# Kernel optimization log

Measured on AMD Instinct MI355X. Metric: run time of the kernel, lower is better.

Reference implementation:

```python
import jax, jax.numpy as jnp
import numpy as np

D_ATT = 256
D_GROUP = 32
N_GROUP = D_ATT // D_GROUP


def setup_inputs() -> dict:
    key = jax.random.key(0)
    ks = jax.random.split(key, 6)
    B, L = 4, 512
    import math
    s = 1.0 / math.sqrt(D_ATT)
    return {
        "x": jax.random.normal(ks[0], (B, L, D_ATT), dtype=jnp.float32),
        "Wq": jax.random.normal(ks[1], (D_ATT, D_ATT), dtype=jnp.float32) * s * 0.06,
        "Wk": jax.random.normal(ks[2], (D_ATT, D_ATT), dtype=jnp.float32) * s * 0.06,
        "Wv": jax.random.normal(ks[3], (D_ATT, D_ATT), dtype=jnp.float32) * s * 0.06,
        "w_mlp": jax.random.normal(ks[4], (D_GROUP,), dtype=jnp.float32) * 0.1,
        "b_mlp": jax.random.normal(ks[5], (1,), dtype=jnp.float32) * 0.1,
    }


def reference(x, Wq, Wk, Wv, w_mlp, b_mlp):
    B, L, d_att = x.shape
    G, Dg = N_GROUP, D_GROUP
    # nn.Linear(bias=False): y = x @ W.T
    Q = x @ Wq.T  # (B, L, d_att)
    K = x @ Wk.T
    V = x @ Wv.T
    Qg = Q.reshape(B, L, 1, G, Dg)
    Kg = K.reshape(B, 1, L, G, Dg)
    # group_MLP: ReLU -> Linear(Dg, 1) -> ReLU, applied to Q-K diff
    # diff: (B, Lq, Lk, G, Dg) -- the huge intermediate a fused kernel would avoid
    diff = Qg - Kg
    attn = jnp.einsum('bqkgd,d->bqkg', jax.nn.relu(diff), w_mlp) + b_mlp[0]
    attn = jax.nn.relu(attn)
    # positional_adding_bias=0, positional_multiplying_bias=1 (defaults), no mask
    attn = jax.nn.softmax(attn, axis=2)  # softmax over key positions
    # NOTE: original views V as (B, L, d_group, n_group) -- asymmetric grouping, kept faithful
    Vg = V.reshape(B, L, Dg, G)
    out = jnp.einsum('bqkg,bkdg->bqdg', attn, Vg)  # (B, Lq, Dg, G)
    return out.reshape(B, L, d_att)
```

## Files before the change

### kernel.cpp

```cpp
#include <hip/hip_runtime.h>

typedef float f32x2 __attribute__((ext_vector_type(2)));
typedef float f32x4 __attribute__((ext_vector_type(4)));
typedef short bf16x8 __attribute__((ext_vector_type(8)));

#define LL 512
#define M_ROWS 2048
#define KC 768

#if __has_builtin(__builtin_amdgcn_exp2f)
#define EXP2F __builtin_amdgcn_exp2f
#else
#define EXP2F exp2f
#endif
#define LOG2E 1.44269504088896340736f

__device__ __forceinline__ float quad_swap1(float x) {
    return __int_as_float(__builtin_amdgcn_mov_dpp(__float_as_int(x), 0xB1, 0xF, 0xF, true));
}
__device__ __forceinline__ float quad_swap2(float x) {
    return __int_as_float(__builtin_amdgcn_mov_dpp(__float_as_int(x), 0x4E, 0xF, 0xF, true));
}

__device__ __forceinline__ unsigned short bf16_rtne(float x) {
    unsigned u = __float_as_uint(x);
    return (unsigned short)((u + 0x7fffu + ((u >> 16) & 1u)) >> 16);
}
__device__ __forceinline__ float bf16_to_f(unsigned short h) {
    return __uint_as_float((unsigned)h << 16);
}

__global__ __launch_bounds__(64) void split_bf16(
    const float* __restrict__ X, const float* __restrict__ Wq,
    const float* __restrict__ Wk, const float* __restrict__ Wv,
    unsigned short* __restrict__ Xc, unsigned short* __restrict__ Wc)
{
    const int row = blockIdx.x;
    const int t = threadIdx.x;
    const float* src;
    unsigned short* hi1; unsigned short* hi2; unsigned short* lo1;
    if (row < M_ROWS) {
        src = X + (size_t)row * 256;
        hi1 = Xc + (size_t)row * KC;
        hi2 = hi1 + 256;
        lo1 = hi1 + 512;
    } else {
        const int n = row - M_ROWS;
        const int mat = n >> 8, c = n & 255;
        const int srow = (mat == 2) ? (((c & 31) << 3) | (c >> 5)) : c;
        src = (mat == 0 ? Wq : (mat == 1 ? Wk : Wv)) + (size_t)srow * 256;
        hi1 = Wc + (size_t)n * KC;
        lo1 = hi1 + 256;
        hi2 = hi1 + 512;
    }
    const f32x4 v = *(const f32x4*)(src + t * 4);
    ushort4 h, l;
    h.x = bf16_rtne(v.x); h.y = bf16_rtne(v.y); h.z = bf16_rtne(v.z); h.w = bf16_rtne(v.w);
    l.x = bf16_rtne(v.x - bf16_to_f(h.x));
    l.y = bf16_rtne(v.y - bf16_to_f(h.y));
    l.z = bf16_rtne(v.z - bf16_to_f(h.z));
    l.w = bf16_rtne(v.w - bf16_to_f(h.w));
    *(ushort4*)(hi1 + t * 4) = h;
    *(ushort4*)(hi2 + t * 4) = h;
    *(ushort4*)(lo1 + t * 4) = l;
}

__global__ __launch_bounds__(64) void qkv_mfma(
    const unsigned short* __restrict__ Xc, const unsigned short* __restrict__ Wc,
    float* __restrict__ Y)
{
    const int bid = blockIdx.x;
    const int m0 = (bid & 31) * 64;
    const int n0 = (bid >> 5) * 64;
    const int l = threadIdx.x;
    const int lr = l & 15;
    const int lk = (l >> 4) * 8;

    size_t aoff[4], boff[4];
#pragma unroll
    for (int i = 0; i < 4; ++i) {
        aoff[i] = (size_t)(m0 + i * 16 + lr) * KC + lk;
        boff[i] = (size_t)(n0 + i * 16 + lr) * KC + lk;
    }

    f32x4 acc[4][4];
#pragma unroll
    for (int i = 0; i < 4; ++i)
#pragma unroll
        for (int j = 0; j < 4; ++j) acc[i][j] = (f32x4){0.f, 0.f, 0.f, 0.f};

    bf16x8 A0[4], B0[4], A1[4], B1[4];
#pragma unroll
    for (int i = 0; i < 4; ++i) {
        A0[i] = *(const bf16x8*)(Xc + aoff[i]);
        B0[i] = *(const bf16x8*)(Wc + boff[i]);
    }

#pragma unroll 1
    for (int it = 0; it < 24; it += 2) {
        const int ks1 = (it + 1) * 32;
#pragma unroll
        for (int i = 0; i < 4; ++i) {
            A1[i] = *(const bf16x8*)(Xc + aoff[i] + ks1);
            B1[i] = *(const bf16x8*)(Wc + boff[i] + ks1);
        }
#pragma unroll
        for (int ai = 0; ai < 4; ++ai)
#pragma unroll
            for (int bi = 0; bi < 4; ++bi)
                acc[ai][bi] = __builtin_amdgcn_mfma_f32_16x16x32_bf16(
                    A0[ai], B0[bi], acc[ai][bi], 0, 0, 0);
        if (it + 2 < 24) {
            const int ks2 = (it + 2) * 32;
#pragma unroll
            for (int i = 0; i < 4; ++i) {
                A0[i] = *(const bf16x8*)(Xc + aoff[i] + ks2);
                B0[i] = *(const bf16x8*)(Wc + boff[i] + ks2);
            }
        }
#pragma unroll
        for (int ai = 0; ai < 4; ++ai)
#pragma unroll
            for (int bi = 0; bi < 4; ++bi)
                acc[ai][bi] = __builtin_amdgcn_mfma_f32_16x16x32_bf16(
                    A1[ai], B1[bi], acc[ai][bi], 0, 0, 0);
    }

    const int mat = n0 >> 8;
    float* Yb = Y + (size_t)mat * M_ROWS * 256;
#pragma unroll
    for (int ai = 0; ai < 4; ++ai)
#pragma unroll
        for (int bi = 0; bi < 4; ++bi) {
            const int col = (n0 & 255) + bi * 16 + lr;
#pragma unroll
            for (int r = 0; r < 4; ++r) {
                const int row = m0 + ai * 16 + (l >> 4) * 4 + r;
                Yb[(size_t)row * 256 + col] = acc[ai][bi][r];
            }
        }
}

__global__ __launch_bounds__(512, 4) void attn_fused(
    const float* __restrict__ Y,
    const float* __restrict__ w_mlp, const float* __restrict__ b_mlp,
    float* __restrict__ out)
{
    const float* Qm = Y;
    const float* Km = Y + (size_t)M_ROWS * 256;
    const float* Vt = Y + (size_t)2 * M_ROWS * 256;

    const int bid = blockIdx.x;
    const int b = bid & 3;
    const int q0 = (bid >> 2) * 4;

    const int t = threadIdx.x;
    const int dh = t & 3;
    const int p = t >> 5;
    const int lane32 = t & 31;
    const int g = lane32 >> 2;

    __shared__ float accbuf[16][32][37];

    const int doff = g * 32 + dh * 8;
    const float bias4 = b_mlp[0] * (LOG2E * 0.25f);

    f32x2 w2[4];
    {
        f32x4 wa = *(const f32x4*)(w_mlp + dh * 8);
        f32x4 wb = *(const f32x4*)(w_mlp + dh * 8 + 4);
        wa *= LOG2E; wb *= LOG2E;
        w2[0] = __builtin_shufflevector(wa, wa, 0, 1);
        w2[1] = __builtin_shufflevector(wa, wa, 2, 3);
        w2[2] = __builtin_shufflevector(wb, wb, 0, 1);
        w2[3] = __builtin_shufflevector(wb, wb, 2, 3);
    }

    f32x2 qr2[4][4];
#pragma unroll
    for (int q = 0; q < 4; ++q) {
        const float* qp = Qm + ((size_t)(b * LL) + q0 + q) * 256 + doff;
        f32x4 qa = *(const f32x4*)qp;
        f32x4 qb = *(const f32x4*)(qp + 4);
        qr2[q][0] = __builtin_shufflevector(qa, qa, 0, 1);
        qr2[q][1] = __builtin_shufflevector(qa, qa, 2, 3);
        qr2[q][2] = __builtin_shufflevector(qb, qb, 0, 1);
        qr2[q][3] = __builtin_shufflevector(qb, qb, 2, 3);
    }

    f32x2 acc2[4][4];
#pragma unroll
    for (int q = 0; q < 4; ++q)
#pragma unroll
        for (int j = 0; j < 4; ++j) acc2[q][j] = (f32x2){0.f, 0.f};
    float l[4] = {0.f, 0.f, 0.f, 0.f};

    const float* kptr = Km + ((size_t)(b * LL) + p) * 256 + doff;
    const float* vptr = Vt + ((size_t)(b * LL) + p) * 256 + doff;

    auto compute = [&](f32x4 ka, f32x4 kb, f32x4 va, f32x4 vb) {
        f32x2 k2[4] = {__builtin_shufflevector(ka, ka, 0, 1),
                       __builtin_shufflevector(ka, ka, 2, 3),
                       __builtin_shufflevector(kb, kb, 0, 1),
                       __builtin_shufflevector(kb, kb, 2, 3)};
        f32x2 v2[4] = {__builtin_shufflevector(va, va, 0, 1),
                       __builtin_shufflevector(va, va, 2, 3),
                       __builtin_shufflevector(vb, vb, 0, 1),
                       __builtin_shufflevector(vb, vb, 2, 3)};
        const f32x2 z2 = {0.f, 0.f};
#pragma unroll
        for (int q = 0; q < 4; ++q) {
            f32x2 s2 = {bias4, 0.f};
#pragma unroll
            for (int j = 0; j < 4; ++j) {
                f32x2 d2 = qr2[q][j] - k2[j];
                f32x2 r2 = __builtin_elementwise_max(d2, z2);
                s2 += w2[j] * r2;
            }
            float s = s2.x + s2.y;
            s += quad_swap1(s);
            s += quad_swap2(s);
            s = fmaxf(s, 0.f);
            const float e = EXP2F(s);
            l[q] += e;
            const f32x2 e2 = {e, e};
#pragma unroll
            for (int j = 0; j < 4; ++j) acc2[q][j] += e2 * v2[j];
        }
    };

    f32x4 ka = *(const f32x4*)kptr, kb = *(const f32x4*)(kptr + 4);
    f32x4 va = *(const f32x4*)vptr, vb = *(const f32x4*)(vptr + 4);
#pragma unroll 1
    for (int i = 0; i < 31; ++i) {
        kptr += 16 * 256; vptr += 16 * 256;
        f32x4 ka2 = *(const f32x4*)kptr, kb2 = *(const f32x4*)(kptr + 4);
        f32x4 va2 = *(const f32x4*)vptr, vb2 = *(const f32x4*)(vptr + 4);
        compute(ka, kb, va, vb);
        ka = ka2; kb = kb2; va = va2; vb = vb2;
    }
    compute(ka, kb, va, vb);

    {
        float* rowp = &accbuf[p][lane32][0];
#pragma unroll
        for (int qq = 0; qq < 4; ++qq)
#pragma unroll
            for (int j = 0; j < 4; ++j)
                *(f32x2*)(rowp + qq * 8 + j * 2) = acc2[qq][j];
        if (dh == 0) {
#pragma unroll
            for (int qq = 0; qq < 4; ++qq) accbuf[p][lane32][32 + qq] = l[qq];
        }
    }
    __syncthreads();

    const int c_o = t & 255;
    const int g_o = c_o & 7, d_o = c_o >> 3;
    const int rowb = g_o * 4 + (d_o >> 3);
    const int colb = d_o & 7;
    const int qsel = t >> 8;
#pragma unroll
    for (int h = 0; h < 2; ++h) {
        const int qh = qsel + 2 * h;
        float s = 0.f, ls = 0.f;
#pragma unroll
        for (int pp = 0; pp < 16; ++pp) {
            s  += accbuf[pp][rowb][qh * 8 + colb];
            ls += accbuf[pp][g_o * 4][32 + qh];
        }
        out[((size_t)(b * LL) + q0 + qh) * 256 + c_o] = s / ls;
    }
}

extern "C" void kernel_launch(void* const* d_in, const int* in_sizes, int n_in,
                              void* d_out, int out_size, void* d_ws, size_t ws_size,
                              hipStream_t stream) {
    (void)in_sizes; (void)n_in; (void)out_size; (void)ws_size;
    const float* x     = (const float*)d_in[0];
    const float* Wq    = (const float*)d_in[1];
    const float* Wk    = (const float*)d_in[2];
    const float* Wv    = (const float*)d_in[3];
    const float* w_mlp = (const float*)d_in[4];
    const float* b_mlp = (const float*)d_in[5];
    float* outp = (float*)d_out;

    float* Y = (float*)d_ws;
    unsigned short* Xc = (unsigned short*)((char*)d_ws + (size_t)6291456);
    unsigned short* Wc = (unsigned short*)((char*)d_ws + (size_t)6291456 + 3145728);

    split_bf16<<<dim3(M_ROWS + 768), 64, 0, stream>>>(x, Wq, Wk, Wv, Xc, Wc);
    qkv_mfma<<<dim3(384), 64, 0, stream>>>(Xc, Wc, Y);
    attn_fused<<<dim3(512), 512, 0, stream>>>(Y, w_mlp, b_mlp, outp);
}
```

Before: 124.3 us.

## Stage K/V tiles through double-buffered shared memory with coalesced loads

Instead of each thread loading its own strided 8-float K/V slices from global memory, the block now cooperatively loads 16-row K and V tiles with coalesced float4 loads into a double-buffered LDS region. The tile is permuted on the way in so that each thread's two float4 reads from LDS are contiguous. The per-thread dimension split changes from 8 consecutive elements to two groups of 4, and the weights, Q and the final reduction indexing are adjusted to match. This adds a __syncthreads per tile and about 64KB of LDS aliased with the accumulation buffer, which may lower occupancy.

```diff
diff --git a/kernel.cpp b/kernel.cpp
--- a/kernel.cpp
+++ b/kernel.cpp
@@ -156,19 +156,24 @@
 
     const int t = threadIdx.x;
     const int dh = t & 3;
-    const int p = t >> 5;
     const int lane32 = t & 31;
     const int g = lane32 >> 2;
-
-    __shared__ float accbuf[16][32][37];
-
-    const int doff = g * 32 + dh * 8;
+    const int p = t >> 5;
+
+    union SMem {
+        struct { float kb[2][16][256]; float vb[2][16][256]; } s;
+        float accbuf[16][32][37];
+    };
+    __shared__ SMem sm;
+
+    const int dA = g * 32 + dh * 4;
+    const int dB = dA + 16;
     const float bias4 = b_mlp[0] * (LOG2E * 0.25f);
 
     f32x2 w2[4];
     {
-        f32x4 wa = *(const f32x4*)(w_mlp + dh * 8);
-        f32x4 wb = *(const f32x4*)(w_mlp + dh * 8 + 4);
+        f32x4 wa = *(const f32x4*)(w_mlp + dh * 4);
+        f32x4 wb = *(const f32x4*)(w_mlp + dh * 4 + 16);
         wa *= LOG2E; wb *= LOG2E;
         w2[0] = __builtin_shufflevector(wa, wa, 0, 1);
         w2[1] = __builtin_shufflevector(wa, wa, 2, 3);
@@ -179,9 +184,9 @@
     f32x2 qr2[4][4];
 #pragma unroll
     for (int q = 0; q < 4; ++q) {
-        const float* qp = Qm + ((size_t)(b * LL) + q0 + q) * 256 + doff;
-        f32x4 qa = *(const f32x4*)qp;
-        f32x4 qb = *(const f32x4*)(qp + 4);
+        const float* qp = Qm + ((size_t)(b * LL) + q0 + q) * 256;
+        f32x4 qa = *(const f32x4*)(qp + dA);
+        f32x4 qb = *(const f32x4*)(qp + dB);
         qr2[q][0] = __builtin_shufflevector(qa, qa, 0, 1);
         qr2[q][1] = __builtin_shufflevector(qa, qa, 2, 3);
         qr2[q][2] = __builtin_shufflevector(qb, qb, 0, 1);
@@ -195,54 +200,87 @@
         for (int j = 0; j < 4; ++j) acc2[q][j] = (f32x2){0.f, 0.f};
     float l[4] = {0.f, 0.f, 0.f, 0.f};
 
-    const float* kptr = Km + ((size_t)(b * LL) + p) * 256 + doff;
-    const float* vptr = Vt + ((size_t)(b * LL) + p) * 256 + doff;
-
-    auto compute = [&](f32x4 ka, f32x4 kb, f32x4 va, f32x4 vb) {
-        f32x2 k2[4] = {__builtin_shufflevector(ka, ka, 0, 1),
-                       __builtin_shufflevector(ka, ka, 2, 3),
-                       __builtin_shufflevector(kb, kb, 0, 1),
-                       __builtin_shufflevector(kb, kb, 2, 3)};
-        f32x2 v2[4] = {__builtin_shufflevector(va, va, 0, 1),
-                       __builtin_shufflevector(va, va, 2, 3),
-                       __builtin_shufflevector(vb, vb, 0, 1),
-                       __builtin_shufflevector(vb, vb, 2, 3)};
-        const f32x2 z2 = {0.f, 0.f};
-#pragma unroll
-        for (int q = 0; q < 4; ++q) {
-            f32x2 s2 = {bias4, 0.f};
-#pragma unroll
-            for (int j = 0; j < 4; ++j) {
-                f32x2 d2 = qr2[q][j] - k2[j];
-                f32x2 r2 = __builtin_elementwise_max(d2, z2);
-                s2 += w2[j] * r2;
+    const float* gsrc[4];
+    float* ldst0[4];
+    float* ldst1[4];
+#pragma unroll
+    for (int r = 0; r < 4; ++r) {
+        const int id = t + 512 * r;
+        const int isv = id >> 10;
+        const int rid = id & 1023;
+        const int row = rid >> 6;
+        const int c = rid & 63;
+        const int gg = c >> 3, c7 = c & 7;
+        const int cp = (c7 < 4) ? (4 * gg + c7) : (28 + 4 * gg + c7);
+        gsrc[r] = (isv ? Vt : Km) + ((size_t)(b * LL) + row) * 256 + 4 * c;
+        ldst0[r] = isv ? &sm.s.vb[0][row][4 * cp] : &sm.s.kb[0][row][4 * cp];
+        ldst1[r] = isv ? &sm.s.vb[1][row][4 * cp] : &sm.s.kb[1][row][4 * cp];
+    }
+
+    {
+        f32x4 st[4];
+#pragma unroll
+        for (int r = 0; r < 4; ++r) st[r] = *(const f32x4*)gsrc[r];
+#pragma unroll
+        for (int r = 0; r < 4; ++r) *(f32x4*)ldst0[r] = st[r];
+    }
+    __syncthreads();
+
+    const f32x2 z2 = {0.f, 0.f};
+#pragma unroll 1
+    for (int tile = 0; tile < 32; ++tile) {
+        const int buf = tile & 1;
+        f32x4 st[4];
+        if (tile < 31) {
+            const size_t adv = (size_t)(tile + 1) * 16 * 256;
+#pragma unroll
+            for (int r = 0; r < 4; ++r) st[r] = *(const f32x4*)(gsrc[r] + adv);
+        }
+        {
+            const float* kr = &sm.s.kb[buf][p][0];
+            const float* vr = &sm.s.vb[buf][p][0];
+            const f32x4 ka = *(const f32x4*)(kr + 4 * lane32);
+            const f32x4 kb_ = *(const f32x4*)(kr + 4 * lane32 + 128);
+            const f32x4 va = *(const f32x4*)(vr + 4 * lane32);
+            const f32x4 vb_ = *(const f32x4*)(vr + 4 * lane32 + 128);
+            f32x2 k2[4] = {__builtin_shufflevector(ka, ka, 0, 1),
+                           __builtin_shufflevector(ka, ka, 2, 3),
+                           __builtin_shufflevector(kb_, kb_, 0, 1),
+                           __builtin_shufflevector(kb_, kb_, 2, 3)};
+            f32x2 v2[4] = {__builtin_shufflevector(va, va, 0, 1),
+                           __builtin_shufflevector(va, va, 2, 3),
+                           __builtin_shufflevector(vb_, vb_, 0, 1),
+                           __builtin_shufflevector(vb_, vb_, 2, 3)};
+#pragma unroll
+            for (int q = 0; q < 4; ++q) {
+                f32x2 s2 = {bias4, 0.f};
+#pragma unroll
+                for (int j = 0; j < 4; ++j) {
+                    f32x2 d2 = qr2[q][j] - k2[j];
+                    f32x2 r2 = __builtin_elementwise_max(d2, z2);
+                    s2 += w2[j] * r2;
+                }
+                float s = s2.x + s2.y;
+                s += quad_swap1(s);
+                s += quad_swap2(s);
+                s = fmaxf(s, 0.f);
+                const float e = EXP2F(s);
+                l[q] += e;
+                const f32x2 e2 = {e, e};
+#pragma unroll
+                for (int j = 0; j < 4; ++j) acc2[q][j] += e2 * v2[j];
             }
-            float s = s2.x + s2.y;
-            s += quad_swap1(s);
-            s += quad_swap2(s);
-            s = fmaxf(s, 0.f);
-            const float e = EXP2F(s);
-            l[q] += e;
-            const f32x2 e2 = {e, e};
-#pragma unroll
-            for (int j = 0; j < 4; ++j) acc2[q][j] += e2 * v2[j];
-        }
-    };
-
-    f32x4 ka = *(const f32x4*)kptr, kb = *(const f32x4*)(kptr + 4);
-    f32x4 va = *(const f32x4*)vptr, vb = *(const f32x4*)(vptr + 4);
-#pragma unroll 1
-    for (int i = 0; i < 31; ++i) {
-        kptr += 16 * 256; vptr += 16 * 256;
-        f32x4 ka2 = *(const f32x4*)kptr, kb2 = *(const f32x4*)(kptr + 4);
-        f32x4 va2 = *(const f32x4*)vptr, vb2 = *(const f32x4*)(vptr + 4);
-        compute(ka, kb, va, vb);
-        ka = ka2; kb = kb2; va = va2; vb = vb2;
-    }
-    compute(ka, kb, va, vb);
+        }
+        if (tile < 31) {
+#pragma unroll
+            for (int r = 0; r < 4; ++r)
+                *(f32x4*)(buf ? ldst0[r] : ldst1[r]) = st[r];
+        }
+        __syncthreads();
+    }
 
     {
-        float* rowp = &accbuf[p][lane32][0];
+        float* rowp = &sm.accbuf[p][lane32][0];
 #pragma unroll
         for (int qq = 0; qq < 4; ++qq)
 #pragma unroll
@@ -250,15 +288,16 @@
                 *(f32x2*)(rowp + qq * 8 + j * 2) = acc2[qq][j];
         if (dh == 0) {
 #pragma unroll
-            for (int qq = 0; qq < 4; ++qq) accbuf[p][lane32][32 + qq] = l[qq];
+            for (int qq = 0; qq < 4; ++qq) sm.accbuf[p][lane32][32 + qq] = l[qq];
         }
     }
     __syncthreads();
 
     const int c_o = t & 255;
-    const int g_o = c_o & 7, d_o = c_o >> 3;
-    const int rowb = g_o * 4 + (d_o >> 3);
-    const int colb = d_o & 7;
+    const int g_o = c_o & 7, dd = c_o >> 3;
+    const int dhp = (dd & 15) >> 2;
+    const int jslot = (dd & 3) + 4 * (dd >> 4);
+    const int rowb = g_o * 4 + dhp;
     const int qsel = t >> 8;
 #pragma unroll
     for (int h = 0; h < 2; ++h) {
@@ -266,8 +305,8 @@
         float s = 0.f, ls = 0.f;
 #pragma unroll
         for (int pp = 0; pp < 16; ++pp) {
-            s  += accbuf[pp][rowb][qh * 8 + colb];
-            ls += accbuf[pp][g_o * 4][32 + qh];
+            s  += sm.accbuf[pp][rowb][qh * 8 + jslot];
+            ls += sm.accbuf[pp][g_o * 4][32 + qh];
         }
         out[((size_t)(b * LL) + q0 + qh) * 256 + c_o] = s / ls;
     }
```

Result: slower. 152.8 us (+22.9%).
